# Optimization experiments

Hardware: AMD Instinct MI355X
Metric: run time of the kernel (lower is better)

## Reference

```python
import jax, jax.numpy as jnp
import numpy as np

B, L = 4, 1024
V, D, H, NL = 32000, 256, 4, 8
S, DC, DI, NTYPES = 16, 4, 512, 5  # d_state, d_conv, d_inner=expand*d_model
NM, NA = 6, 2  # mamba blocks (layers 0,1,2,4,5,6), attention blocks (layers 3,7)


def layernorm(x, g, b):
    m = x.mean(-1, keepdims=True)
    v = x.var(-1, keepdims=True)
    return (x - m) / jnp.sqrt(v + 1e-5) * g + b


def mamba_block(x, g, b, in_w, conv_w, conv_b, xproj_w, dt_w, dt_b, A_log, Dp, out_w):
    res = x
    xn = layernorm(x, g, b)
    xz = xn @ in_w.T                          # [B,L,2*DI]
    xb, z = jnp.split(xz, 2, axis=-1)
    # depthwise causal conv1d (torch pads both sides then truncates to L == left-pad only)
    xc = jnp.transpose(xb, (0, 2, 1))         # [B,DI,L]
    xc = jax.lax.conv_general_dilated(xc, conv_w, (1,), [(DC - 1, 0)], feature_group_count=DI)
    xc = xc + conv_b[None, :, None]
    xb = jax.nn.silu(jnp.transpose(xc, (0, 2, 1)))  # [B,L,DI]
    A = -jnp.exp(A_log)                        # [DI,S]
    Bm, Cm = jnp.split(xb @ xproj_w.T, 2, axis=-1)  # each [B,L,S]
    dt = jax.nn.softplus(xb @ dt_w.T + dt_b)   # [B,L,DI]

    def step(h, inp):
        dt_t, B_t, C_t, x_t = inp              # [B,DI],[B,S],[B,S],[B,DI]
        A_bar = jnp.exp(dt_t[:, :, None] * A)  # [B,DI,S]
        h = A_bar * h + (dt_t * x_t)[:, :, None] * B_t[:, None, :]
        y = (h * C_t[:, None, :]).sum(-1) + Dp * x_t
        return h, y

    h0 = jnp.zeros((x.shape[0], DI, S), x.dtype)
    xs = (jnp.swapaxes(dt, 0, 1), jnp.swapaxes(Bm, 0, 1), jnp.swapaxes(Cm, 0, 1), jnp.swapaxes(xb, 0, 1))
    _, ys = jax.lax.scan(step, h0, xs)         # ys: [L,B,DI]
    y = jnp.swapaxes(ys, 0, 1) * jax.nn.silu(z)
    return y @ out_w.T + res


def attn_block(x, ts, mask, g, b, qkv_w, out_w, decay, ffg, ffb, ff1, ff2):
    Bs, Lq, Dm = x.shape
    dh = Dm // H
    res = x
    xn = layernorm(x, g, b)
    qkv = (xn @ qkv_w.T).reshape(Bs, Lq, 3, H, dh)
    q, k, v = qkv[:, :, 0], qkv[:, :, 1], qkv[:, :, 2]   # [B,L,H,dh]
    attn = jnp.einsum('bqhd,bkhd->bhqk', q, k) * dh ** -0.5
    t_diff = jnp.abs(ts[:, :, None] - ts[:, None, :])[:, None] / 24.0   # [B,1,L,L]
    attn = attn - jax.nn.softplus(decay)[None, :, None, None] * t_diff
    causal = jnp.triu(jnp.ones((Lq, Lq), bool), 1)
    attn = jnp.where(causal[None, None], -jnp.inf, attn)
    attn = jnp.where((mask == 0)[:, None, None, :], -jnp.inf, attn)
    attn = jax.nn.softmax(attn, axis=-1)       # dropout inactive (eval)
    out = jnp.einsum('bhqk,bkhd->bqhd', attn, v).reshape(Bs, Lq, Dm)
    x = res + out @ out_w.T
    xn2 = layernorm(x, ffg, ffb)
    return x + jax.nn.silu(xn2 @ ff1.T) @ ff2.T


def setup_inputs():
    key = jax.random.key(0)
    ks = iter(jax.random.split(key, 64))
    rn = lambda shape, s=0.02: jax.random.normal(next(ks), shape, jnp.float32) * s
    A_init = jnp.log(jnp.tile(jnp.arange(1, S + 1, dtype=jnp.float32)[None, None, :], (NM, DI, 1)))
    return dict(
        token_ids=jax.random.randint(next(ks), (B, L), 0, V, jnp.int32),
        token_types=jax.random.randint(next(ks), (B, L), 0, NTYPES, jnp.int32),
        timestamps=jax.random.uniform(next(ks), (B, L), jnp.float32) * 100.0,
        attention_mask=jnp.ones((B, L), jnp.int32),
        tok_emb=rn((V, D)).at[0].set(0.0),  # padding_idx=0
        type_emb=rn((NTYPES, D)),
        te_freq=rn((D // 2,), 0.01), te_phase=jnp.zeros((D // 2,)),
        te_w=rn((D, D)), te_b=jnp.zeros((D,)),
        m_norm_g=jnp.ones((NM, D)), m_norm_b=jnp.zeros((NM, D)),
        m_in_w=rn((NM, 2 * DI, D)),
        m_conv_w=rn((NM, DI, 1, DC)), m_conv_b=jnp.zeros((NM, DI)),
        m_xproj_w=rn((NM, 2 * S, DI)),
        m_dt_w=rn((NM, DI, DI)), m_dt_b=jnp.zeros((NM, DI)),
        m_Alog=A_init, m_D=jnp.ones((NM, DI)),
        m_out_w=rn((NM, D, DI)),
        a_norm_g=jnp.ones((NA, D)), a_norm_b=jnp.zeros((NA, D)),
        a_qkv_w=rn((NA, 3 * D, D)), a_out_w=rn((NA, D, D)),
        a_decay=jnp.full((NA, H), 0.01, jnp.float32),
        a_ffg=jnp.ones((NA, D)), a_ffb=jnp.zeros((NA, D)),
        a_ff1=rn((NA, 4 * D, D)), a_ff2=rn((NA, D, 4 * D)),
        f_g=jnp.ones((D,)), f_b=jnp.zeros((D,)),
        lm_w=rn((V, D)),
        re_w=rn((1, D)), re_b=jnp.zeros((1,)),
        mo_w=rn((1, D)), mo_b=jnp.zeros((1,)),
    )


def reference(token_ids, token_types, timestamps, attention_mask,
              tok_emb, type_emb, te_freq, te_phase, te_w, te_b,
              m_norm_g, m_norm_b, m_in_w, m_conv_w, m_conv_b, m_xproj_w,
              m_dt_w, m_dt_b, m_Alog, m_D, m_out_w,
              a_norm_g, a_norm_b, a_qkv_w, a_out_w, a_decay, a_ffg, a_ffb, a_ff1, a_ff2,
              f_g, f_b, lm_w, re_w, re_b, mo_w, mo_b):
    t = timestamps[..., None]
    freq = jax.nn.softplus(te_freq)
    enc = jnp.concatenate([jnp.sin(t * freq + te_phase), jnp.cos(t * freq + te_phase)], -1) @ te_w.T + te_b
    x = tok_emb[token_ids] + type_emb[token_types] + enc
    mi = ai = 0
    for i in range(NL):
        if (i + 1) % 4 == 0:
            x = attn_block(x, timestamps, attention_mask,
                           a_norm_g[ai], a_norm_b[ai], a_qkv_w[ai], a_out_w[ai], a_decay[ai],
                           a_ffg[ai], a_ffb[ai], a_ff1[ai], a_ff2[ai])
            ai += 1
        else:
            x = mamba_block(x, m_norm_g[mi], m_norm_b[mi], m_in_w[mi], m_conv_w[mi], m_conv_b[mi],
                            m_xproj_w[mi], m_dt_w[mi], m_dt_b[mi], m_Alog[mi], m_D[mi], m_out_w[mi])
            mi += 1
    x = layernorm(x, f_g, f_b)
    cls = x[:, 0, :]
    lm_logits = x @ lm_w.T
    readm = (cls @ re_w.T + re_b)[:, 0]
    mort = (cls @ mo_w.T + mo_b)[:, 0]
    return lm_logits, readm, mort
```

## Files before the change

kernel.cpp:

```cpp
#include <hip/hip_runtime.h>
#include <hip/hip_bf16.h>
#include <math.h>

#define BB 4
#define LL 1024
#define BL (BB*LL)
#define DD 256
#define VV 32000
#define HH 4
#define DH 64
#define SS 16
#define DCC 4
#define DII 512

typedef float f32x4 __attribute__((ext_vector_type(4)));
typedef short bh8  __attribute__((ext_vector_type(8)));
typedef unsigned short u16;

__device__ __forceinline__ float sp_f(float x) {
    return fmaxf(x, 0.f) + log1pf(expf(-fabsf(x)));
}
__device__ __forceinline__ float silu_f(float x) {
    return x / (1.f + expf(-x));
}
__device__ __forceinline__ short f2bf(float f) {
    __hip_bfloat16 h = __float2bfloat16(f);
    short s; __builtin_memcpy(&s, &h, 2); return s;
}
__device__ __forceinline__ float bf2f(u16 u) {
    unsigned v = ((unsigned)u) << 16;
    float f; __builtin_memcpy(&f, &v, 4); return f;
}

#define WB_TOT 5668864
#define LM_TOT 8192000
__global__ void cvtall_k(const float* __restrict__ te_w, const float* __restrict__ a_qkv,
                         const float* __restrict__ a_out, const float* __restrict__ a_ff1,
                         const float* __restrict__ a_ff2, const float* __restrict__ m_in,
                         const float* __restrict__ m_out, const float* __restrict__ m_dt,
                         const float* __restrict__ m_xp, const float* __restrict__ lm,
                         u16* __restrict__ dst, u16* __restrict__ dlm) {
    long i = ((long)blockIdx.x * 256 + threadIdx.x) * 4;
    const float* src; long off; u16* d; long doff;
    if (i >= WB_TOT) {
        long j = i - WB_TOT;
        if (j >= LM_TOT) return;
        src = lm; off = j; d = dlm; doff = j;
    } else {
        d = dst; doff = i;
        if      (i < 65536)   { src = te_w;  off = i; }
        else if (i < 458752)  { src = a_qkv; off = i - 65536; }
        else if (i < 589824)  { src = a_out; off = i - 458752; }
        else if (i < 1114112) { src = a_ff1; off = i - 589824; }
        else if (i < 1638400) { src = a_ff2; off = i - 1114112; }
        else if (i < 3211264) { src = m_in;  off = i - 1638400; }
        else if (i < 3997696) { src = m_out; off = i - 3211264; }
        else {
            long l = i - 3997696;
            int mi = (int)(l / 278528);
            long r = l - (long)mi * 278528;
            if (r < 262144) { src = m_dt + (long)mi * 262144; off = r; }
            else            { src = m_xp + (long)mi * 16384;  off = r - 262144; }
        }
    }
    float4 v = *(const float4*)(src + off);
    ushort4 u;
    u.x = (u16)f2bf(v.x); u.y = (u16)f2bf(v.y);
    u.z = (u16)f2bf(v.z); u.w = (u16)f2bf(v.w);
    *(ushort4*)(d + doff) = u;
}

__global__ void feat_k(const float* __restrict__ ts, const float* __restrict__ freq,
                       const float* __restrict__ phase, u16* __restrict__ feat) {
    int row = blockIdx.x, t = threadIdx.x;
    float tv = ts[row];
    int d = t & 127;
    float f = sp_f(freq[d]);
    float arg = tv * f + phase[d];
    feat[(size_t)row * DD + t] = (u16)f2bf((t < 128) ? sinf(arg) : cosf(arg));
}

__global__ void ln_k(const float* __restrict__ x, const float* __restrict__ g,
                     const float* __restrict__ bbias, u16* __restrict__ out) {
    __shared__ float red[8];
    int row = blockIdx.x, t = threadIdx.x;
    float v = x[(size_t)row * DD + t];
    float s = v;
    #pragma unroll
    for (int o = 32; o >= 1; o >>= 1) s += __shfl_xor(s, o);
    if ((t & 63) == 0) red[t >> 6] = s;
    __syncthreads();
    float mean = (red[0] + red[1] + red[2] + red[3]) * (1.f / 256.f);
    float d = v - mean;
    float s2 = d * d;
    #pragma unroll
    for (int o = 32; o >= 1; o >>= 1) s2 += __shfl_xor(s2, o);
    if ((t & 63) == 0) red[4 + (t >> 6)] = s2;
    __syncthreads();
    float var = (red[4] + red[5] + red[6] + red[7]) * (1.f / 256.f);
    out[(size_t)row * DD + t] = (u16)f2bf(d * rsqrtf(var + 1e-5f) * g[t] + bbias[t]);
}

template <int ACT, bool BOUT, bool VT>
__global__ __launch_bounds__(256) void lngemm_k(
    const float* __restrict__ X, const float* __restrict__ g, const float* __restrict__ bb,
    const u16* __restrict__ W, void* __restrict__ outv, u16* __restrict__ vt,
    int M, int N) {
    __shared__ __align__(16) char Abf[32768];
    __shared__ __align__(16) char Ws[8192];
    __shared__ float gs[256], bs[256];
    int tid = threadIdx.x;
    int bm = blockIdx.y * 64, bn = blockIdx.x * 64;
    gs[tid] = g[tid]; bs[tid] = bb[tid];

    int row = tid >> 2, part = tid & 3;
    const float* xr = X + (size_t)(bm + row) * 256 + part * 64;
    float4 vv[16];
    float s = 0.f, sq = 0.f;
    #pragma unroll
    for (int i = 0; i < 16; ++i) {
        vv[i] = *(const float4*)(xr + i * 4);
        s  += vv[i].x + vv[i].y + vv[i].z + vv[i].w;
        sq += vv[i].x * vv[i].x + vv[i].y * vv[i].y + vv[i].z * vv[i].z + vv[i].w * vv[i].w;
    }
    s += __shfl_xor(s, 1);  s += __shfl_xor(s, 2);
    sq += __shfl_xor(sq, 1); sq += __shfl_xor(sq, 2);
    float mean = s * (1.f / 256.f);
    float rstd = rsqrtf(sq * (1.f / 256.f) - mean * mean + 1e-5f);
    __syncthreads();
    #pragma unroll
    for (int i8 = 0; i8 < 8; ++i8) {
        bh8 p;
        #pragma unroll
        for (int j = 0; j < 8; ++j) {
            int e = i8 * 8 + j;
            float v = (j & 3) == 0 ? vv[e >> 2].x : (j & 3) == 1 ? vv[e >> 2].y
                    : (j & 3) == 2 ? vv[e >> 2].z : vv[e >> 2].w;
            int c = part * 64 + e;
            p[j] = f2bf((v - mean) * rstd * gs[c] + bs[c]);
        }
        *(bh8*)(Abf + (unsigned)((row * 512 + part * 128 + i8 * 16) ^ ((row & 7) << 4))) = p;
    }
    __syncthreads();

    int lane = tid & 63, wv = tid >> 6;
    int wm = wv >> 1, wn = wv & 1;
    int ro = lane & 15, kg = lane >> 4;
    f32x4 acc[2][2];
    #pragma unroll
    for (int i = 0; i < 2; ++i)
        #pragma unroll
        for (int j = 0; j < 2; ++j) acc[i][j] = (f32x4){0.f, 0.f, 0.f, 0.f};

    const u16* gw = W + (size_t)(bn + row) * 256 + part * 16;
    bool wvalid = (bn + row) < N;
    unsigned swb = (unsigned)(row * 128 + part * 32);
    unsigned sx  = (unsigned)((row & 7) << 4);
    for (int kk = 0; kk < 256; kk += 64) {
        if (kk) __syncthreads();
        bh8 w0 = {}, w1 = {};
        if (wvalid) { w0 = *(const bh8*)(gw + kk); w1 = *(const bh8*)(gw + kk + 8); }
        *(bh8*)(Ws + (swb ^ sx)) = w0;
        *(bh8*)(Ws + ((swb + 16) ^ sx)) = w1;
        __syncthreads();
        #pragma unroll
        for (int ks = 0; ks < 2; ++ks) {
            bh8 af[2], bf_[2];
            #pragma unroll
            for (int m = 0; m < 2; ++m) {
                int r = wm * 32 + m * 16 + ro;
                af[m] = *(const bh8*)(Abf + (unsigned)((r * 512 + kk * 2 + ks * 64 + kg * 16) ^ ((r & 7) << 4)));
            }
            #pragma unroll
            for (int n = 0; n < 2; ++n) {
                int r = wn * 32 + n * 16 + ro;
                bf_[n] = *(const bh8*)(Ws + (unsigned)((r * 128 + ks * 64 + kg * 16) ^ ((r & 7) << 4)));
            }
            #pragma unroll
            for (int m = 0; m < 2; ++m)
                #pragma unroll
                for (int n = 0; n < 2; ++n)
                    acc[m][n] = __builtin_amdgcn_mfma_f32_16x16x32_bf16(af[m], bf_[n], acc[m][n], 0, 0, 0);
        }
    }

    float* outf = (float*)outv;
    u16*   outb = (u16*)outv;
    int cr = (lane >> 4) * 4, cc = lane & 15;
    #pragma unroll
    for (int mf = 0; mf < 2; ++mf) {
        #pragma unroll
        for (int nf = 0; nf < 2; ++nf) {
            int n = bn + wn * 32 + nf * 16 + cc;
            if (n >= N) continue;
            int mbase = bm + wm * 32 + mf * 16 + cr;
            f32x4 a = acc[mf][nf];
            #pragma unroll
            for (int r = 0; r < 4; ++r) {
                float v = a[r];
                if (ACT == 1) v = silu_f(v);
                if (BOUT) outb[(size_t)(mbase + r) * N + n] = (u16)f2bf(v);
                else      outf[(size_t)(mbase + r) * N + n] = v;
            }
            if (VT && n >= 512) {
                int hh = (n - 512) >> 6, dd = (n - 512) & 63;
                int b_ = mbase >> 10, l = mbase & 1023;
                ushort4 uv;
                uv.x = (u16)f2bf(acc[mf][nf][0]); uv.y = (u16)f2bf(acc[mf][nf][1]);
                uv.z = (u16)f2bf(acc[mf][nf][2]); uv.w = (u16)f2bf(acc[mf][nf][3]);
                *(ushort4*)(vt + ((((size_t)b_ * HH + hh) * DH + dd) << 10) + l) = uv;
            }
        }
    }
}

template <int ACT, bool HASB, bool HASR, bool BOUT>
__global__ __launch_bounds__(256) void bgemm_k(
    const u16* __restrict__ A, const u16* __restrict__ W,
    const float* __restrict__ bias, const float* __restrict__ res,
    void* __restrict__ outv, float* __restrict__ out2, int M, int N, int K) {
    __shared__ __align__(16) char lds[16384];
    char* As = lds;
    char* Ws = lds + 8192;
    int tid = threadIdx.x;
    int bm = blockIdx.y * 64, bn = blockIdx.x * 64;
    int row = tid >> 2, q = tid & 3;
    int lane = tid & 63, wv = tid >> 6;
    int wm = wv >> 1, wn = wv & 1;
    int ro = lane & 15, kg = lane >> 4;

    f32x4 acc[2][2];
    #pragma unroll
    for (int i = 0; i < 2; ++i)
        #pragma unroll
        for (int j = 0; j < 2; ++j) acc[i][j] = (f32x4){0.f, 0.f, 0.f, 0.f};

    const u16* ga = A + (size_t)(bm + row) * K + q * 16;
    const u16* gw = W + (size_t)(bn + row) * K + q * 16;
    bool wvalid = (bn + row) < N;
    unsigned swb = (unsigned)(row * 128 + q * 32);
    unsigned sx  = (unsigned)((row & 7) << 4);

    for (int kk = 0; kk < K; kk += 64) {
        if (kk) __syncthreads();
        {
            *(bh8*)(As + (swb ^ sx)) = *(const bh8*)(ga);
            *(bh8*)(As + ((swb + 16) ^ sx)) = *(const bh8*)(ga + 8);
            bh8 w0 = {}, w1 = {};
            if (wvalid) { w0 = *(const bh8*)(gw); w1 = *(const bh8*)(gw + 8); }
            *(bh8*)(Ws + (swb ^ sx)) = w0;
            *(bh8*)(Ws + ((swb + 16) ^ sx)) = w1;
        }
        ga += 64; gw += 64;
        __syncthreads();
        #pragma unroll
        for (int ks = 0; ks < 2; ++ks) {
            bh8 af[2], bf_[2];
            #pragma unroll
            for (int m = 0; m < 2; ++m) {
                int r = wm * 32 + m * 16 + ro;
                af[m] = *(const bh8*)(As + (unsigned)((r * 128 + ks * 64 + kg * 16) ^ ((r & 7) << 4)));
            }
            #pragma unroll
            for (int n = 0; n < 2; ++n) {
                int r = wn * 32 + n * 16 + ro;
                bf_[n] = *(const bh8*)(Ws + (unsigned)((r * 128 + ks * 64 + kg * 16) ^ ((r & 7) << 4)));
            }
            #pragma unroll
            for (int m = 0; m < 2; ++m)
                #pragma unroll
                for (int n = 0; n < 2; ++n)
                    acc[m][n] = __builtin_amdgcn_mfma_f32_16x16x32_bf16(af[m], bf_[n], acc[m][n], 0, 0, 0);
        }
    }

    float* outf = (float*)outv;
    u16*   outb = (u16*)outv;
    int cr = (lane >> 4) * 4, cc = lane & 15;
    #pragma unroll
    for (int mf = 0; mf < 2; ++mf) {
        #pragma unroll
        for (int nf = 0; nf < 2; ++nf) {
            int n = bn + wn * 32 + nf * 16 + cc;
            if (n >= N) continue;
            int mbase = bm + wm * 32 + mf * 16 + cr;
            f32x4 a = acc[mf][nf];
            #pragma unroll
            for (int r = 0; r < 4; ++r) {
                float v = a[r];
                int m = mbase + r;
                if (ACT == 3) {
                    if (n < 512) outf[(size_t)m * 512 + n] = sp_f(v + bias[n]);
                    else         out2[(size_t)m * 32 + (n - 512)] = v;
                } else {
                    if (HASB) v += bias[n];
                    if (ACT == 1) v = silu_f(v);
                    if (HASR) v += res[(size_t)m * N + n];
                    if (BOUT) outb[(size_t)m * N + n] = (u16)f2bf(v);
                    else      outf[(size_t)m * N + n] = v;
                }
            }
        }
    }
}

template <int ACT, bool HASB, bool HASR>
__global__ __launch_bounds__(256) void bgemm32_k(
    const u16* __restrict__ A, const u16* __restrict__ W,
    const float* __restrict__ bias, const float* __restrict__ res,
    float* __restrict__ out, int M, int N, int K,
    const int* __restrict__ ids, const int* __restrict__ typ,
    const float* __restrict__ tok, const float* __restrict__ tpe) {
    __shared__ __align__(16) char As[4096];
    __shared__ __align__(16) char Ws[8192];
    int tid = threadIdx.x;
    int bm = blockIdx.y * 32, bn = blockIdx.x * 64;
    int lane = tid & 63, wv = tid >> 6;
    int wm = wv >> 1, wn = wv & 1;
    int ro = lane & 15, kg = lane >> 4;

    f32x4 acc[2];
    acc[0] = (f32x4){0.f, 0.f, 0.f, 0.f};
    acc[1] = (f32x4){0.f, 0.f, 0.f, 0.f};

    int arow = tid >> 3, aq = tid & 7;
    const u16* ga = A + (size_t)(bm + arow) * K + aq * 8;
    unsigned aswb = (unsigned)(arow * 128 + aq * 16);
    unsigned asx  = (unsigned)((arow & 7) << 4);
    int wrow = tid >> 2, wq = tid & 3;
    const u16* gw = W + (size_t)(bn + wrow) * K + wq * 16;
    unsigned wswb = (unsigned)(wrow * 128 + wq * 32);
    unsigned wsx  = (unsigned)((wrow & 7) << 4);

    for (int kk = 0; kk < K; kk += 64) {
        if (kk) __syncthreads();
        *(bh8*)(As + (aswb ^ asx)) = *(const bh8*)(ga);
        *(bh8*)(Ws + (wswb ^ wsx)) = *(const bh8*)(gw);
        *(bh8*)(Ws + ((wswb + 16) ^ wsx)) = *(const bh8*)(gw + 8);
        ga += 64; gw += 64;
        __syncthreads();
        #pragma unroll
        for (int ks = 0; ks < 2; ++ks) {
            int r = wm * 16 + ro;
            bh8 af = *(const bh8*)(As + (unsigned)((r * 128 + ks * 64 + kg * 16) ^ ((r & 7) << 4)));
            #pragma unroll
            for (int n = 0; n < 2; ++n) {
                int rr = wn * 32 + n * 16 + ro;
                bh8 bf_ = *(const bh8*)(Ws + (unsigned)((rr * 128 + ks * 64 + kg * 16) ^ ((rr & 7) << 4)));
                acc[n] = __builtin_amdgcn_mfma_f32_16x16x32_bf16(af, bf_, acc[n], 0, 0, 0);
            }
        }
    }

    int cr = (lane >> 4) * 4, cc = lane & 15;
    #pragma unroll
    for (int nf = 0; nf < 2; ++nf) {
        int n = bn + wn * 32 + nf * 16 + cc;
        int mbase = bm + wm * 16 + cr;
        #pragma unroll
        for (int r = 0; r < 4; ++r) {
            float v = acc[nf][r];
            int m = mbase + r;
            if (ACT == 4) {
                v += bias[n] + tok[(size_t)ids[m] * DD + n] + tpe[(size_t)typ[m] * DD + n];
            } else {
                if (HASB) v += bias[n];
                if (HASR) v += res[(size_t)m * N + n];
            }
            out[(size_t)m * N + n] = v;
        }
    }
}

__global__ __launch_bounds__(256) void mgemmL_k(
    const u16* __restrict__ A, const u16* __restrict__ W,
    float* __restrict__ out, int M, int N, int K) {
    __shared__ __align__(16) char lds[32768];
    char* As = lds;
    char* Ws = lds + 16384;
    int lid = blockIdx.y * 32 + blockIdx.x;
    int xcd = lid & 7, wk = lid >> 3;
    int nt = xcd * 32 + (wk >> 5);
    int mt = wk & 31;
    if (nt * 128 >= N) return;
    int bm = mt * 128, bn = nt * 128;

    int tid = threadIdx.x;
    int row = tid >> 1, half = tid & 1;
    int lane = tid & 63, wv = tid >> 6;
    int wm = wv >> 1, wn = wv & 1;
    int ro = lane & 15, kg = lane >> 4;

    f32x4 acc[4][4];
    #pragma unroll
    for (int i = 0; i < 4; ++i)
        #pragma unroll
        for (int j = 0; j < 4; ++j) acc[i][j] = (f32x4){0.f, 0.f, 0.f, 0.f};

    const u16* ga = A + (size_t)(bm + row) * K + half * 32;
    const u16* gw = W + (size_t)(bn + row) * K + half * 32;
    unsigned swb = (unsigned)(row * 128 + half * 64);
    unsigned sx  = (unsigned)((row & 7) << 4);

    for (int kk = 0; kk < K; kk += 64) {
        if (kk) __syncthreads();
        #pragma unroll
        for (int j = 0; j < 4; ++j) {
            *(bh8*)(As + ((swb + j * 16) ^ sx)) = *(const bh8*)(ga + j * 8);
            *(bh8*)(Ws + ((swb + j * 16) ^ sx)) = *(const bh8*)(gw + j * 8);
        }
        ga += 64; gw += 64;
        __syncthreads();
        #pragma unroll
        for (int ks = 0; ks < 2; ++ks) {
            bh8 af[4], bf_[4];
            #pragma unroll
            for (int m = 0; m < 4; ++m) {
                int r = wm * 64 + m * 16 + ro;
                af[m] = *(const bh8*)(As + (unsigned)((r * 128 + ks * 64 + kg * 16) ^ ((r & 7) << 4)));
            }
            #pragma unroll
            for (int n = 0; n < 4; ++n) {
                int r = wn * 64 + n * 16 + ro;
                bf_[n] = *(const bh8*)(Ws + (unsigned)((r * 128 + ks * 64 + kg * 16) ^ ((r & 7) << 4)));
            }
            #pragma unroll
            for (int m = 0; m < 4; ++m)
                #pragma unroll
                for (int n = 0; n < 4; ++n)
                    acc[m][n] = __builtin_amdgcn_mfma_f32_16x16x32_bf16(af[m], bf_[n], acc[m][n], 0, 0, 0);
        }
    }

    int cr = (lane >> 4) * 4, cc = lane & 15;
    #pragma unroll
    for (int mf = 0; mf < 4; ++mf) {
        #pragma unroll
        for (int nf = 0; nf < 4; ++nf) {
            int n = bn + wn * 64 + nf * 16 + cc;
            int mbase = bm + wm * 64 + mf * 16 + cr;
            f32x4 a = acc[mf][nf];
            #pragma unroll
            for (int r = 0; r < 4; ++r)
                out[(size_t)(mbase + r) * N + n] = a[r];
        }
    }
}

__global__ void conv_k(const u16* __restrict__ xz, const float* __restrict__ w,
                       const float* __restrict__ cb, u16* __restrict__ xbb) {
    int idx = blockIdx.x * blockDim.x + threadIdx.x;
    int c = idx & (DII - 1);
    int row = idx >> 9;
    int l = row & (LL - 1);
    int base = row - l;
    const float* wc = w + c * DCC;
    float s = cb[c];
    #pragma unroll
    for (int j = 0; j < DCC; ++j) {
        int ll = l - (DCC - 1) + j;
        if (ll >= 0) s = fmaf(wc[j], bf2f(xz[((size_t)(base + ll)) * (2 * DII) + c]), s);
    }
    xbb[(size_t)idx] = (u16)f2bf(silu_f(s));
}

__global__ __launch_bounds__(256) void scan_k(
    const float* __restrict__ dt, const u16* __restrict__ xb,
    const float* __restrict__ bc, const u16* __restrict__ xz,
    const float* __restrict__ Alog, const float* __restrict__ Dp,
    u16* __restrict__ y) {
    __shared__ float pa[SS][257];
    __shared__ float ph[SS][257];
    int di = blockIdx.x & (DII - 1);
    int b  = blockIdx.x >> 9;
    int t  = threadIdx.x;
    int l0 = t * 4;
    size_t rb = (size_t)(b * LL + l0);

    float A[SS];
    #pragma unroll
    for (int s = 0; s < SS; ++s) A[s] = -expf(Alog[di * SS + s]);

    float dtv[4], xv[4];
    #pragma unroll
    for (int j = 0; j < 4; ++j) {
        dtv[j] = dt[(rb + j) * DII + di];
        xv[j]  = bf2f(xb[(rb + j) * DII + di]);
    }

    float Pa[SS], Ph[SS];
    #pragma unroll
    for (int j = 0; j < 4; ++j) {
        float u = dtv[j] * xv[j];
        const float* bt = bc + (rb + j) * (2 * SS);
        #pragma unroll
        for (int s = 0; s < SS; ++s) {
            float a = expf(dtv[j] * A[s]);
            float w = u * bt[s];
            if (j == 0) { Pa[s] = a; Ph[s] = w; }
            else        { Pa[s] *= a; Ph[s] = fmaf(a, Ph[s], w); }
        }
    }
    #pragma unroll
    for (int s = 0; s < SS; ++s) { pa[s][t] = Pa[s]; ph[s][t] = Ph[s]; }
    __syncthreads();

    #pragma unroll
    for (int off = 1; off < 256; off <<= 1) {
        float qa[SS], qh[SS];
        bool has = (t >= off);
        if (has) {
            #pragma unroll
            for (int s = 0; s < SS; ++s) { qa[s] = pa[s][t - off]; qh[s] = ph[s][t - off]; }
        }
        __syncthreads();
        if (has) {
            #pragma unroll
            for (int s = 0; s < SS; ++s) {
                ph[s][t] = fmaf(pa[s][t], qh[s], ph[s][t]);
                pa[s][t] *= qa[s];
            }
        }
        __syncthreads();
    }

    float h[SS];
    if (t == 0) {
        #pragma unroll
        for (int s = 0; s < SS; ++s) h[s] = 0.f;
    } else {
        #pragma unroll
        for (int s = 0; s < SS; ++s) h[s] = ph[s][t - 1];
    }
    float Dv = Dp[di];
    #pragma unroll
    for (int j = 0; j < 4; ++j) {
        float u = dtv[j] * xv[j];
        const float* bt = bc + (rb + j) * (2 * SS);
        float acc = 0.f;
        #pragma unroll
        for (int s = 0; s < SS; ++s) {
            float a = expf(dtv[j] * A[s]);
            h[s] = fmaf(a, h[s], u * bt[s]);
            acc = fmaf(h[s], bt[SS + s], acc);
        }
        float zv = bf2f(xz[(rb + j) * (2 * DII) + DII + di]);
        y[(rb + j) * DII + di] = (u16)f2bf(fmaf(Dv, xv[j], acc) * silu_f(zv));
    }
}

__global__ __launch_bounds__(512) void fattn_k(
    const u16* __restrict__ qkv, const u16* __restrict__ vt,
    const float* __restrict__ ts, const int* __restrict__ mask,
    const float* __restrict__ decay, u16* __restrict__ out) {
    __shared__ __align__(16) char ksm[2][8192];
    __shared__ __align__(16) char vsm[2][8192];
    __shared__ __align__(16) char psm[16384];
    __shared__ float mrg[256][25];
    __shared__ float tsk[2][64];
    __shared__ int   msk[2][64];

    int tid = threadIdx.x;
    int grp = tid >> 8;
    int lt  = tid & 255;
    int lane = tid & 63;
    int wvi = (tid >> 6) & 3;
    int qt = blockIdx.x & 15;
    int h  = (blockIdx.x >> 4) & 3;
    int b  = blockIdx.x >> 6;
    int q0 = qt * 64;
    int g = lane >> 4, c = lane & 15;

    bh8 qf[2];
    {
        const u16* qrow = qkv + ((size_t)(b * LL + q0 + wvi * 16 + c)) * (3 * DD) + h * DH;
        qf[0] = *(const bh8*)(qrow + g * 8);
        qf[1] = *(const bh8*)(qrow + 32 + g * 8);
    }
    float tq[4];
    #pragma unroll
    for (int j = 0; j < 4; ++j) tq[j] = ts[b * LL + q0 + wvi * 16 + g * 4 + j];
    float spd = sp_f(decay[h]);

    f32x4 o[4];
    #pragma unroll
    for (int n = 0; n < 4; ++n) o[n] = (f32x4){0.f, 0.f, 0.f, 0.f};
    float mrow[4] = {-INFINITY, -INFINITY, -INFINITY, -INFINITY};
    float drow[4] = {0.f, 0.f, 0.f, 0.f};

    char* pw = psm + (tid >> 6) * 2048;

    int nt = (qt + 2) >> 1;
    for (int it = 0; it < nt; ++it) {
        int kt = it * 2 + grp;
        bool act = (kt <= qt);
        int k0 = kt * 64;
        __syncthreads();
        if (act) {
            int row = lt >> 2, qq = lt & 3;
            unsigned sw = (unsigned)((row & 7) << 4);
            unsigned base = (unsigned)(row * 128 + qq * 32);
            const u16* kr = qkv + ((size_t)(b * LL + k0 + row)) * (3 * DD) + DD + h * DH + qq * 16;
            *(bh8*)(ksm[grp] + (base ^ sw)) = *(const bh8*)(kr);
            *(bh8*)(ksm[grp] + ((base + 16) ^ sw)) = *(const bh8*)(kr + 8);
            const u16* vr = vt + ((((size_t)b * HH + h) * DH + row) << 10) + k0 + qq * 16;
            *(bh8*)(vsm[grp] + (base ^ sw)) = *(const bh8*)(vr);
            *(bh8*)(vsm[grp] + ((base + 16) ^ sw)) = *(const bh8*)(vr + 8);
            if (lt < 64) { tsk[grp][lt] = ts[b * LL + k0 + lt]; msk[grp][lt] = mask[b * LL + k0 + lt]; }
        }
        __syncthreads();
        if (!act) continue;

        f32x4 sf[4];
        #pragma unroll
        for (int n = 0; n < 4; ++n) sf[n] = (f32x4){0.f, 0.f, 0.f, 0.f};
        #pragma unroll
        for (int ks = 0; ks < 2; ++ks) {
            #pragma unroll
            for (int nf = 0; nf < 4; ++nf) {
                int rr = nf * 16 + c;
                bh8 kf = *(const bh8*)(ksm[grp] + (unsigned)((rr * 128 + ks * 64 + g * 16) ^ ((rr & 7) << 4)));
                sf[nf] = __builtin_amdgcn_mfma_f32_16x16x32_bf16(qf[ks], kf, sf[nf], 0, 0, 0);
            }
        }
        float mnew[4] = {mrow[0], mrow[1], mrow[2], mrow[3]};
        #pragma unroll
        for (int nf = 0; nf < 4; ++nf) {
            int kk = c + 16 * nf;
            float tk = tsk[grp][kk];
            bool md = (msk[grp][kk] == 0);
            #pragma unroll
            for (int j = 0; j < 4; ++j) {
                int qrow = q0 + wvi * 16 + g * 4 + j;
                float s = sf[nf][j] * 0.125f - spd * fabsf(tq[j] - tk) * (1.f / 24.f);
                bool dead = md || (k0 + kk > qrow);
                s = dead ? -INFINITY : s;
                sf[nf][j] = s;
                mnew[j] = fmaxf(mnew[j], s);
            }
        }
        #pragma unroll
        for (int off = 1; off <= 8; off <<= 1)
            #pragma unroll
            for (int j = 0; j < 4; ++j) mnew[j] = fmaxf(mnew[j], __shfl_xor(mnew[j], off));
        float scl[4], psum[4];
        #pragma unroll
        for (int j = 0; j < 4; ++j) {
            scl[j] = (mnew[j] == -INFINITY) ? 1.f : expf(mrow[j] - mnew[j]);
            psum[j] = 0.f;
            mrow[j] = mnew[j];
        }
        #pragma unroll
        for (int nf = 0; nf < 4; ++nf) {
            #pragma unroll
            for (int j = 0; j < 4; ++j) {
                float s = sf[nf][j];
                float p = (s == -INFINITY) ? 0.f : expf(s - mrow[j]);
                psum[j] += p;
                int row = g * 4 + j;
                *(short*)(pw + (unsigned)((row * 128 + (c + 16 * nf) * 2) ^ ((row & 7) << 4))) = f2bf(p);
            }
        }
        #pragma unroll
        for (int off = 1; off <= 8; off <<= 1)
            #pragma unroll
            for (int j = 0; j < 4; ++j) psum[j] += __shfl_xor(psum[j], off);
        #pragma unroll
        for (int j = 0; j < 4; ++j) drow[j] = drow[j] * scl[j] + psum[j];
        #pragma unroll
        for (int n = 0; n < 4; ++n)
            #pragma unroll
            for (int j = 0; j < 4; ++j) o[n][j] *= scl[j];
        #pragma unroll
        for (int ks = 0; ks < 2; ++ks) {
            bh8 pf = *(const bh8*)(pw + (unsigned)((c * 128 + ks * 64 + g * 16) ^ ((c & 7) << 4)));
            #pragma unroll
            for (int n = 0; n < 4; ++n) {
                int rr = n * 16 + c;
                bh8 vf = *(const bh8*)(vsm[grp] + (unsigned)((rr * 128 + ks * 64 + g * 16) ^ ((rr & 7) << 4)));
                o[n] = __builtin_amdgcn_mfma_f32_16x16x32_bf16(pf, vf, o[n], 0, 0, 0);
            }
        }
    }

    __syncthreads();
    if (grp == 1) {
        float* m_ = mrg[lt];
        #pragma unroll
        for (int j = 0; j < 4; ++j) { m_[j] = mrow[j]; m_[4 + j] = drow[j]; }
        #pragma unroll
        for (int n = 0; n < 4; ++n)
            #pragma unroll
            for (int j = 0; j < 4; ++j) m_[8 + n * 4 + j] = o[n][j];
    }
    __syncthreads();
    if (grp == 0) {
        float* m_ = mrg[lt];
        #pragma unroll
        for (int j = 0; j < 4; ++j) {
            float m1 = m_[j], d1 = m_[4 + j];
            float mm = fmaxf(mrow[j], m1);
            float s0 = (mrow[j] == -INFINITY) ? 0.f : expf(mrow[j] - mm);
            float s1 = (m1 == -INFINITY) ? 0.f : expf(m1 - mm);
            drow[j] = drow[j] * s0 + d1 * s1;
            #pragma unroll
            for (int n = 0; n < 4; ++n)
                o[n][j] = o[n][j] * s0 + m_[8 + n * 4 + j] * s1;
        }
        #pragma unroll
        for (int n = 0; n < 4; ++n) {
            #pragma unroll
            for (int j = 0; j < 4; ++j) {
                int qrow = q0 + wvi * 16 + g * 4 + j;
                out[((size_t)(b * LL + qrow)) * DD + h * DH + c + 16 * n] = (u16)f2bf(o[n][j] / drow[j]);
            }
        }
    }
}

__global__ __launch_bounds__(64) void heads_k(
    const u16* __restrict__ xn, const float* __restrict__ re_w, const float* __restrict__ re_b,
    const float* __restrict__ mo_w, const float* __restrict__ mo_b, float* __restrict__ out) {
    int lane = threadIdx.x;
    int b = blockIdx.x & 3;
    int which = blockIdx.x >> 2;
    const float* wv = which ? mo_w : re_w;
    const u16* row = xn + (size_t)b * LL * DD;
    float s = 0.f;
    #pragma unroll
    for (int d = 0; d < DD / 64; ++d) s = fmaf(bf2f(row[lane + d * 64]), wv[lane + d * 64], s);
    #pragma unroll
    for (int o = 32; o >= 1; o >>= 1) s += __shfl_xor(s, o);
    if (lane == 0) out[(size_t)VV * BL + which * 4 + b] = s + (which ? mo_b[0] : re_b[0]);
}

extern "C" void kernel_launch(void* const* d_in, const int* in_sizes, int n_in,
                              void* d_out, int out_size, void* d_ws, size_t ws_size,
                              hipStream_t stream) {
    const int*   ids      = (const int*)  d_in[0];
    const int*   typ      = (const int*)  d_in[1];
    const float* ts       = (const float*)d_in[2];
    const int*   amask    = (const int*)  d_in[3];
    const float* tok_emb  = (const float*)d_in[4];
    const float* type_emb = (const float*)d_in[5];
    const float* te_freq  = (const float*)d_in[6];
    const float* te_phase = (const float*)d_in[7];
    const float* te_w     = (const float*)d_in[8];
    const float* te_b     = (const float*)d_in[9];
    const float* m_norm_g = (const float*)d_in[10];
    const float* m_norm_b = (const float*)d_in[11];
    const float* m_in_w   = (const float*)d_in[12];
    const float* m_conv_w = (const float*)d_in[13];
    const float* m_conv_b = (const float*)d_in[14];
    const float* m_xproj  = (const float*)d_in[15];
    const float* m_dt_w   = (const float*)d_in[16];
    const float* m_dt_b   = (const float*)d_in[17];
    const float* m_Alog   = (const float*)d_in[18];
    const float* m_D      = (const float*)d_in[19];
    const float* m_out_w  = (const float*)d_in[20];
    const float* a_norm_g = (const float*)d_in[21];
    const float* a_norm_b = (const float*)d_in[22];
    const float* a_qkv_w  = (const float*)d_in[23];
    const float* a_out_w  = (const float*)d_in[24];
    const float* a_decay  = (const float*)d_in[25];
    const float* a_ffg    = (const float*)d_in[26];
    const float* a_ffb    = (const float*)d_in[27];
    const float* a_ff1    = (const float*)d_in[28];
    const float* a_ff2    = (const float*)d_in[29];
    const float* f_g      = (const float*)d_in[30];
    const float* f_b      = (const float*)d_in[31];
    const float* lm_w     = (const float*)d_in[32];
    const float* re_w     = (const float*)d_in[33];
    const float* re_b     = (const float*)d_in[34];
    const float* mo_w     = (const float*)d_in[35];
    const float* mo_b     = (const float*)d_in[36];

    float* out = (float*)d_out;
    float* ws  = (float*)d_ws;

    float* x    = ws;
    u16*   xnb  = (u16*)(ws + 1048576);
    u16*   t1   = (u16*)(ws + 1572864);
    u16*   b1   = (u16*)(ws + 3670016);
    u16*   b2   = (u16*)(ws + 5767168);
    float* t3   = ws + 6815744;
    float* t5   = ws + 8912896;
    u16*   vtb  = (u16*)(ws + 9043968);
    u16*   wbuf = (u16*)(ws + 9568256);
    u16*   wlm  = (u16*)(ws + 12402688);

    const u16* w_te  = wbuf;
    const u16* w_qkv = wbuf + 65536;
    const u16* w_ao  = wbuf + 458752;
    const u16* w_ff1 = wbuf + 589824;
    const u16* w_ff2 = wbuf + 1114112;
    const u16* w_min = wbuf + 1638400;
    const u16* w_mo  = wbuf + 3211264;
    const u16* w_dtx = wbuf + 3997696;

    cvtall_k<<<(WB_TOT + LM_TOT) / 1024, 256, 0, stream>>>(
        te_w, a_qkv_w, a_out_w, a_ff1, a_ff2, m_in_w, m_out_w, m_dt_w, m_xproj, lm_w, wbuf, wlm);
    feat_k<<<BL, 256, 0, stream>>>(ts, te_freq, te_phase, b1);
    bgemm32_k<4, true, false><<<dim3(4, BL / 32), 256, 0, stream>>>(
        b1, w_te, te_b, nullptr, x, BL, DD, DD, ids, typ, tok_emb, type_emb);

    int mi = 0, ai = 0;
    for (int i = 0; i < 8; ++i) {
        if ((i + 1) % 4 == 0) {
            lngemm_k<0, true, true><<<dim3(12, BL / 64), 256, 0, stream>>>(
                x, a_norm_g + ai * DD, a_norm_b + ai * DD,
                w_qkv + (size_t)ai * 196608, t1, vtb, BL, 3 * DD);
            fattn_k<<<BB * HH * (LL / 64), 512, 0, stream>>>(
                t1, vtb, ts, amask, a_decay + ai * HH, b1);
            bgemm32_k<0, false, true><<<dim3(4, BL / 32), 256, 0, stream>>>(
                b1, w_ao + (size_t)ai * 65536, nullptr, x, x, BL, DD, DD,
                nullptr, nullptr, nullptr, nullptr);
            lngemm_k<1, true, false><<<dim3(16, BL / 64), 256, 0, stream>>>(
                x, a_ffg + ai * DD, a_ffb + ai * DD,
                w_ff1 + (size_t)ai * 262144, b1, nullptr, BL, 4 * DD);
            bgemm32_k<0, false, true><<<dim3(4, BL / 32), 256, 0, stream>>>(
                b1, w_ff2 + (size_t)ai * 262144, nullptr, x, x, BL, DD, 4 * DD,
                nullptr, nullptr, nullptr, nullptr);
            ++ai;
        } else {
            lngemm_k<0, true, false><<<dim3(16, BL / 64), 256, 0, stream>>>(
                x, m_norm_g + mi * DD, m_norm_b + mi * DD,
                w_min + (size_t)mi * 262144, t1, nullptr, BL, 2 * DII);
            conv_k<<<(BL * DII) / 256, 256, 0, stream>>>(
                t1, m_conv_w + (size_t)mi * DII * DCC, m_conv_b + mi * DII, b1);
            bgemm_k<3, true, false, false><<<dim3(9, BL / 64), 256, 0, stream>>>(
                b1, w_dtx + (size_t)mi * 278528, m_dt_b + mi * DII, nullptr, t3, t5, BL, 544, DII);
            scan_k<<<BB * DII, 256, 0, stream>>>(
                t3, b1, t5, t1, m_Alog + (size_t)mi * DII * SS, m_D + mi * DII, b2);
            bgemm32_k<0, false, true><<<dim3(4, BL / 32), 256, 0, stream>>>(
                b2, w_mo + (size_t)mi * 131072, nullptr, x, x, BL, DD, DII,
                nullptr, nullptr, nullptr, nullptr);
            ++mi;
        }
    }

    ln_k<<<BL, 256, 0, stream>>>(x, f_g, f_b, xnb);
    mgemmL_k<<<dim3(32, 256), 256, 0, stream>>>(xnb, wlm, out, BL, VV, DD);
    heads_k<<<8, 64, 0, stream>>>(xnb, re_w, re_b, mo_w, mo_b, out);
}
```

Before: 1.372 ms.

## Stage GEMM and attention tiles via direct global-to-LDS loads

Replaces the register-staged global→LDS copies in all the bf16 GEMM kernels and the flash-attention K/V loads with global_load_lds 16-byte transfers that write straight into shared memory. The XOR swizzle moves from the LDS address to the global source column, so each wave fills a contiguous 1KB chunk of eight rows. This removes the VGPR round trip and the ds_write instructions, but the N-bound guard on W rows is dropped. It also relies on the compiler inserting the right waits before the barriers.

```diff
diff --git a/kernel.cpp b/kernel.cpp
--- a/kernel.cpp
+++ b/kernel.cpp
@@ -30,6 +30,12 @@
 __device__ __forceinline__ float bf2f(u16 u) {
     unsigned v = ((unsigned)u) << 16;
     float f; __builtin_memcpy(&f, &v, 4); return f;
+}
+
+__device__ __forceinline__ void gll16(const u16* g, void* l) {
+    __builtin_amdgcn_global_load_lds(
+        (const __attribute__((address_space(1))) void*)g,
+        (__attribute__((address_space(3))) void*)l, 16, 0, 0);
 }
 
 #define WB_TOT 5668864
@@ -141,27 +147,25 @@
         }
         *(bh8*)(Abf + (unsigned)((row * 512 + part * 128 + i8 * 16) ^ ((row & 7) << 4))) = p;
     }
-    __syncthreads();
 
     int lane = tid & 63, wv = tid >> 6;
     int wm = wv >> 1, wn = wv & 1;
     int ro = lane & 15, kg = lane >> 4;
+    int swe = (((lane & 7) ^ (lane >> 3)) * 8);
+    int lrow8 = lane >> 3;
     f32x4 acc[2][2];
     #pragma unroll
     for (int i = 0; i < 2; ++i)
         #pragma unroll
         for (int j = 0; j < 2; ++j) acc[i][j] = (f32x4){0.f, 0.f, 0.f, 0.f};
 
-    const u16* gw = W + (size_t)(bn + row) * 256 + part * 16;
-    bool wvalid = (bn + row) < N;
-    unsigned swb = (unsigned)(row * 128 + part * 32);
-    unsigned sx  = (unsigned)((row & 7) << 4);
     for (int kk = 0; kk < 256; kk += 64) {
         if (kk) __syncthreads();
-        bh8 w0 = {}, w1 = {};
-        if (wvalid) { w0 = *(const bh8*)(gw + kk); w1 = *(const bh8*)(gw + kk + 8); }
-        *(bh8*)(Ws + (swb ^ sx)) = w0;
-        *(bh8*)(Ws + ((swb + 16) ^ sx)) = w1;
+        #pragma unroll
+        for (int ch = wv; ch < 8; ch += 4) {
+            int r = ch * 8 + lrow8;
+            gll16(W + (size_t)(bn + r) * 256 + kk + swe, Ws + ch * 1024);
+        }
         __syncthreads();
         #pragma unroll
         for (int ks = 0; ks < 2; ++ks) {
@@ -219,39 +223,30 @@
     const u16* __restrict__ A, const u16* __restrict__ W,
     const float* __restrict__ bias, const float* __restrict__ res,
     void* __restrict__ outv, float* __restrict__ out2, int M, int N, int K) {
-    __shared__ __align__(16) char lds[16384];
-    char* As = lds;
-    char* Ws = lds + 8192;
+    __shared__ __align__(16) char As[8192];
+    __shared__ __align__(16) char Ws[8192];
     int tid = threadIdx.x;
     int bm = blockIdx.y * 64, bn = blockIdx.x * 64;
-    int row = tid >> 2, q = tid & 3;
     int lane = tid & 63, wv = tid >> 6;
     int wm = wv >> 1, wn = wv & 1;
     int ro = lane & 15, kg = lane >> 4;
+    int swe = (((lane & 7) ^ (lane >> 3)) * 8);
+    int lrow8 = lane >> 3;
 
     f32x4 acc[2][2];
     #pragma unroll
     for (int i = 0; i < 2; ++i)
         #pragma unroll
         for (int j = 0; j < 2; ++j) acc[i][j] = (f32x4){0.f, 0.f, 0.f, 0.f};
-
-    const u16* ga = A + (size_t)(bm + row) * K + q * 16;
-    const u16* gw = W + (size_t)(bn + row) * K + q * 16;
-    bool wvalid = (bn + row) < N;
-    unsigned swb = (unsigned)(row * 128 + q * 32);
-    unsigned sx  = (unsigned)((row & 7) << 4);
 
     for (int kk = 0; kk < K; kk += 64) {
         if (kk) __syncthreads();
-        {
-            *(bh8*)(As + (swb ^ sx)) = *(const bh8*)(ga);
-            *(bh8*)(As + ((swb + 16) ^ sx)) = *(const bh8*)(ga + 8);
-            bh8 w0 = {}, w1 = {};
-            if (wvalid) { w0 = *(const bh8*)(gw); w1 = *(const bh8*)(gw + 8); }
-            *(bh8*)(Ws + (swb ^ sx)) = w0;
-            *(bh8*)(Ws + ((swb + 16) ^ sx)) = w1;
-        }
-        ga += 64; gw += 64;
+        #pragma unroll
+        for (int ch = wv; ch < 8; ch += 4) {
+            int r = ch * 8 + lrow8;
+            gll16(A + (size_t)(bm + r) * K + kk + swe, As + ch * 1024);
+            gll16(W + (size_t)(bn + r) * K + kk + swe, Ws + ch * 1024);
+        }
         __syncthreads();
         #pragma unroll
         for (int ks = 0; ks < 2; ++ks) {
@@ -318,26 +313,24 @@
     int lane = tid & 63, wv = tid >> 6;
     int wm = wv >> 1, wn = wv & 1;
     int ro = lane & 15, kg = lane >> 4;
+    int swe = (((lane & 7) ^ (lane >> 3)) * 8);
+    int lrow8 = lane >> 3;
 
     f32x4 acc[2];
     acc[0] = (f32x4){0.f, 0.f, 0.f, 0.f};
     acc[1] = (f32x4){0.f, 0.f, 0.f, 0.f};
 
-    int arow = tid >> 3, aq = tid & 7;
-    const u16* ga = A + (size_t)(bm + arow) * K + aq * 8;
-    unsigned aswb = (unsigned)(arow * 128 + aq * 16);
-    unsigned asx  = (unsigned)((arow & 7) << 4);
-    int wrow = tid >> 2, wq = tid & 3;
-    const u16* gw = W + (size_t)(bn + wrow) * K + wq * 16;
-    unsigned wswb = (unsigned)(wrow * 128 + wq * 32);
-    unsigned wsx  = (unsigned)((wrow & 7) << 4);
-
     for (int kk = 0; kk < K; kk += 64) {
         if (kk) __syncthreads();
-        *(bh8*)(As + (aswb ^ asx)) = *(const bh8*)(ga);
-        *(bh8*)(Ws + (wswb ^ wsx)) = *(const bh8*)(gw);
-        *(bh8*)(Ws + ((wswb + 16) ^ wsx)) = *(const bh8*)(gw + 8);
-        ga += 64; gw += 64;
+        {
+            int r = wv * 8 + lrow8;
+            gll16(A + (size_t)(bm + r) * K + kk + swe, As + wv * 1024);
+            #pragma unroll
+            for (int ch = wv; ch < 8; ch += 4) {
+                int rw = ch * 8 + lrow8;
+                gll16(W + (size_t)(bn + rw) * K + kk + swe, Ws + ch * 1024);
+            }
+        }
         __syncthreads();
         #pragma unroll
         for (int ks = 0; ks < 2; ++ks) {
@@ -375,9 +368,8 @@
 __global__ __launch_bounds__(256) void mgemmL_k(
     const u16* __restrict__ A, const u16* __restrict__ W,
     float* __restrict__ out, int M, int N, int K) {
-    __shared__ __align__(16) char lds[32768];
-    char* As = lds;
-    char* Ws = lds + 16384;
+    __shared__ __align__(16) char As[16384];
+    __shared__ __align__(16) char Ws[16384];
     int lid = blockIdx.y * 32 + blockIdx.x;
     int xcd = lid & 7, wk = lid >> 3;
     int nt = xcd * 32 + (wk >> 5);
@@ -386,30 +378,26 @@
     int bm = mt * 128, bn = nt * 128;
 
     int tid = threadIdx.x;
-    int row = tid >> 1, half = tid & 1;
     int lane = tid & 63, wv = tid >> 6;
     int wm = wv >> 1, wn = wv & 1;
     int ro = lane & 15, kg = lane >> 4;
+    int swe = (((lane & 7) ^ (lane >> 3)) * 8);
+    int lrow8 = lane >> 3;
 
     f32x4 acc[4][4];
     #pragma unroll
     for (int i = 0; i < 4; ++i)
         #pragma unroll
         for (int j = 0; j < 4; ++j) acc[i][j] = (f32x4){0.f, 0.f, 0.f, 0.f};
-
-    const u16* ga = A + (size_t)(bm + row) * K + half * 32;
-    const u16* gw = W + (size_t)(bn + row) * K + half * 32;
-    unsigned swb = (unsigned)(row * 128 + half * 64);
-    unsigned sx  = (unsigned)((row & 7) << 4);
 
     for (int kk = 0; kk < K; kk += 64) {
         if (kk) __syncthreads();
         #pragma unroll
-        for (int j = 0; j < 4; ++j) {
-            *(bh8*)(As + ((swb + j * 16) ^ sx)) = *(const bh8*)(ga + j * 8);
-            *(bh8*)(Ws + ((swb + j * 16) ^ sx)) = *(const bh8*)(gw + j * 8);
-        }
-        ga += 64; gw += 64;
+        for (int ch = wv; ch < 16; ch += 4) {
+            int r = ch * 8 + lrow8;
+            gll16(A + (size_t)(bm + r) * K + kk + swe, As + ch * 1024);
+            gll16(W + (size_t)(bn + r) * K + kk + swe, Ws + ch * 1024);
+        }
         __syncthreads();
         #pragma unroll
         for (int ks = 0; ks < 2; ++ks) {
@@ -564,12 +552,15 @@
     int grp = tid >> 8;
     int lt  = tid & 255;
     int lane = tid & 63;
-    int wvi = (tid >> 6) & 3;
+    int wgrp = (tid >> 6) & 3;
+    int wvi = wgrp;
     int qt = blockIdx.x & 15;
     int h  = (blockIdx.x >> 4) & 3;
     int b  = blockIdx.x >> 6;
     int q0 = qt * 64;
     int g = lane >> 4, c = lane & 15;
+    int swe = (((lane & 7) ^ (lane >> 3)) * 8);
+    int lrow8 = lane >> 3;
 
     bh8 qf[2];
     {
@@ -597,15 +588,14 @@
         int k0 = kt * 64;
         __syncthreads();
         if (act) {
-            int row = lt >> 2, qq = lt & 3;
-            unsigned sw = (unsigned)((row & 7) << 4);
-            unsigned base = (unsigned)(row * 128 + qq * 32);
-            const u16* kr = qkv + ((size_t)(b * LL + k0 + row)) * (3 * DD) + DD + h * DH + qq * 16;
-            *(bh8*)(ksm[grp] + (base ^ sw)) = *(const bh8*)(kr);
-            *(bh8*)(ksm[grp] + ((base + 16) ^ sw)) = *(const bh8*)(kr + 8);
-            const u16* vr = vt + ((((size_t)b * HH + h) * DH + row) << 10) + k0 + qq * 16;
-            *(bh8*)(vsm[grp] + (base ^ sw)) = *(const bh8*)(vr);
-            *(bh8*)(vsm[grp] + ((base + 16) ^ sw)) = *(const bh8*)(vr + 8);
+            #pragma unroll
+            for (int ch = wgrp; ch < 8; ch += 4) {
+                int r = ch * 8 + lrow8;
+                gll16(qkv + ((size_t)(b * LL + k0 + r)) * (3 * DD) + DD + h * DH + swe,
+                      ksm[grp] + ch * 1024);
+                gll16(vt + ((((size_t)b * HH + h) * DH + r) << 10) + k0 + swe,
+                      vsm[grp] + ch * 1024);
+            }
             if (lt < 64) { tsk[grp][lt] = ts[b * LL + k0 + lt]; msk[grp][lt] = mask[b * LL + k0 + lt]; }
         }
         __syncthreads();
```

Result: no change. 1.397 ms (+1.8%).
